# Performance work log

Measured on AMD Instinct MI355X. Metric: run time of the kernel, lower is better.

## Reference

```python
import jax, jax.numpy as jnp
import numpy as np

KSIZE = 11
SIGMA = 1.5
WEIGHTS = (0.0448, 0.2856, 0.3001, 0.2363, 0.1333)  # Wang et al. 2003
K1, K2 = 0.01, 0.03
DATA_RANGE = 1.0


def _gaussian_kernel():
    x = jnp.arange(KSIZE, dtype=jnp.float32) - KSIZE // 2
    k = jnp.exp(-x ** 2 / (2.0 * SIGMA ** 2))
    return k / k.sum()


def _filt(x, k1d):
    # Depthwise 2D Gaussian as two separable 1D depthwise convs (outer-product
    # kernel + zero padding => identical to the torch 2D conv with padding=5).
    C = x.shape[1]
    pad = KSIZE // 2
    dn = ('NCHW', 'OIHW', 'NCHW')
    kh = jnp.tile(k1d.reshape(1, 1, KSIZE, 1), (C, 1, 1, 1))
    kw = jnp.tile(k1d.reshape(1, 1, 1, KSIZE), (C, 1, 1, 1))
    x = jax.lax.conv_general_dilated(x, kh, (1, 1), [(pad, pad), (0, 0)],
                                     dimension_numbers=dn, feature_group_count=C)
    x = jax.lax.conv_general_dilated(x, kw, (1, 1), [(0, 0), (pad, pad)],
                                     dimension_numbers=dn, feature_group_count=C)
    return x


def _ssim_per_channel(img1, img2, k1d):
    C1 = (K1 * DATA_RANGE) ** 2
    C2 = (K2 * DATA_RANGE) ** 2
    mu1 = _filt(img1, k1d)
    mu2 = _filt(img2, k1d)
    mu1_sq = mu1 * mu1
    mu2_sq = mu2 * mu2
    mu12 = mu1 * mu2
    sigma1_sq = _filt(img1 * img1, k1d) - mu1_sq
    sigma2_sq = _filt(img2 * img2, k1d) - mu2_sq
    sigma12 = _filt(img1 * img2, k1d) - mu12
    cs_map = (2.0 * sigma12 + C2) / (sigma1_sq + sigma2_sq + C2)
    ssim_map = (2.0 * mu12 + C1) / (mu1_sq + mu2_sq + C1) * cs_map
    return ssim_map.mean(axis=(2, 3)), cs_map.mean(axis=(2, 3))  # (B, C) each


def _avg_pool2(x):
    B, C, H, W = x.shape
    return x.reshape(B, C, H // 2, 2, W // 2, 2).mean(axis=(3, 5))


def setup_inputs() -> dict:
    key = jax.random.key(0)
    k1, k2 = jax.random.split(key)
    img1 = jax.random.uniform(k1, (16, 3, 512, 512), dtype=jnp.float32)
    img2 = jax.random.uniform(k2, (16, 3, 512, 512), dtype=jnp.float32)
    return {"img1": img1, "img2": img2}


def reference(img1, img2):
    weights = jnp.array(WEIGHTS, dtype=jnp.float32)
    k1d = _gaussian_kernel()
    x1 = img1.astype(jnp.float32)
    x2 = img2.astype(jnp.float32)
    levels = len(WEIGHTS)
    mcs = []
    for i in range(levels):
        ssim_c, cs_c = _ssim_per_channel(x1, x2, k1d)
        if i < levels - 1:
            mcs.append(cs_c.mean(axis=1))
            x1 = _avg_pool2(x1)
            x2 = _avg_pool2(x2)
        else:
            mcs.append(ssim_c.mean(axis=1))
    mcs = jnp.clip(jnp.stack(mcs, axis=1), 0.0, None)  # (B, levels)
    ms_ssim_val = (mcs ** weights[None, :]).prod(axis=1)  # (B,)
    return ms_ssim_val.mean()
```

## Files before the change

### kernel.cpp

```cpp
#include <hip/hip_runtime.h>

#define NT 256

typedef float v2f __attribute__((ext_vector_type(2)));
typedef float f4u __attribute__((ext_vector_type(4), aligned(4)));

__device__ __forceinline__ constexpr float Wj(int j) {
    return (j < 0 || j > 10) ? 0.f :
           (j == 0 || j == 10) ? 0.00102838f :
           (j == 1 || j == 9)  ? 0.00759878f :
           (j == 2 || j == 8)  ? 0.03600077f :
           (j == 3 || j == 7)  ? 0.10936069f :
           (j == 4 || j == 6)  ? 0.21300553f : 0.26601172f;
}

__global__ __attribute__((amdgpu_flat_work_group_size(NT, NT), amdgpu_waves_per_eu(2, 4)))
void msssim_slide_kernel(
    const float* __restrict__ x1, const float* __restrict__ x2, int strideIn,
    float* __restrict__ p1, float* __restrict__ p2, int strideOut,
    float* __restrict__ accCS, float* __restrict__ accSSIM,
    int H, int W, int strips, int chunksY, int chunkRows, int padded)
{
    const int t = threadIdx.x;
    const int lane = t & 63;

    const int cpx = gridDim.x >> 3;
    const int lb = (blockIdx.x & 7) * cpx + (blockIdx.x >> 3);
    const int wid = lb * (NT / 64) + (t >> 6);

    const int perImg = strips * chunksY;
    const int img = wid / perImg;
    const int rem = wid - img * perImg;
    const int strip = rem / chunksY;
    const int chunk = rem % chunksY;
    const int cc = strip * 64 + lane;
    const int r0 = chunk * chunkRows;
    const int hEnd = r0 + chunkRows + 5;
    const bool edge = (!padded) && (strip == 0 || strip == strips - 1);
    const bool laneValid = (cc < W);
    const bool doPool = (p1 != nullptr);
    const int Wp = W >> 1;

    const size_t imgIn = (size_t)img * H * strideIn;
    const float* __restrict__ base1 = x1 + imgIn;
    const float* __restrict__ base2 = x2 + imgIn;
    const size_t imgOut = doPool ? (size_t)img * (H >> 1) * strideOut : 0;
    float* __restrict__ q1 = doPool ? (p1 + imgOut) : nullptr;
    float* __restrict__ q2 = doPool ? (p2 + imgOut) : nullptr;

    float nx1[12], nx2[12];
    v2f psd[11], psq[11];
    float prs1 = 0.f, prs2 = 0.f;
    float cs_s = 0.f, ssim_s = 0.f;

    auto loadRow = [&](int h) {
        if (h < 0 || h >= H || !laneValid) return;
        const float* __restrict__ r1 = base1 + (size_t)h * strideIn;
        const float* __restrict__ r2 = base2 + (size_t)h * strideIn;
        if (!edge) {
            const f4u* a4 = reinterpret_cast<const f4u*>(r1 + (cc - 5));
            const f4u* b4 = reinterpret_cast<const f4u*>(r2 + (cc - 5));
            f4u A0 = a4[0], A1 = a4[1], A2 = a4[2];
            f4u B0 = b4[0], B1 = b4[1], B2 = b4[2];
#pragma unroll
            for (int j = 0; j < 4; ++j) { nx1[j] = A0[j]; nx1[4 + j] = A1[j]; nx1[8 + j] = A2[j]; }
#pragma unroll
            for (int j = 0; j < 4; ++j) { nx2[j] = B0[j]; nx2[4 + j] = B1[j]; nx2[8 + j] = B2[j]; }
        } else {
#pragma unroll
            for (int j = 0; j < 12; ++j) {
                int col = cc + j - 5;
                int cl = col < 0 ? 0 : (col > W - 1 ? W - 1 : col);
                float a = r1[cl], b = r2[cl];
                bool ok = (col >= 0) && (col < W);
                nx1[j] = ok ? a : 0.f;
                nx2[j] = ok ? b : 0.f;
            }
        }
    };

    loadRow(r0 - 5);

    const float C1 = 0.0001f, C2 = 0.0009f;

    for (int hb = r0 - 5; hb < hEnd; hb += 11) {
#pragma unroll
        for (int p = 0; p < 11; ++p) {
            const int h = hb + p;
            if (h < hEnd) {
                v2f acc_sd = (v2f){0.f, 0.f}, acc_sq = (v2f){0.f, 0.f};
                const bool rv = (h >= 0) && (h < H);
                if (rv) {
                    if (doPool && h >= r0 && h < r0 + chunkRows) {
                        float ra = nx1[5] + nx1[6];
                        float rb = nx2[5] + nx2[6];
                        if ((h & 1) == 0) { prs1 = ra; prs2 = rb; }
                        else if (!(lane & 1) && laneValid) {
                            size_t po = (size_t)(h >> 1) * strideOut + (cc >> 1);
                            q1[po] = 0.25f * (prs1 + ra);
                            q2[po] = 0.25f * (prs2 + rb);
                            if (cc == 0) {
                                *(f4u*)&q1[po - 8] = (f4u){0.f, 0.f, 0.f, 0.f};
                                *(f4u*)&q1[po - 4] = (f4u){0.f, 0.f, 0.f, 0.f};
                                *(f4u*)&q2[po - 8] = (f4u){0.f, 0.f, 0.f, 0.f};
                                *(f4u*)&q2[po - 4] = (f4u){0.f, 0.f, 0.f, 0.f};
                            }
                            if ((cc >> 1) == Wp - 1) {
#pragma unroll
                                for (int j = 1; j <= 8; ++j) { q1[po + j] = 0.f; q2[po + j] = 0.f; }
                            }
                        }
                    }
#pragma unroll
                    for (int j = 0; j < 11; ++j) {
                        float s = nx1[j] + nx2[j];
                        float d = nx1[j] - nx2[j];
                        v2f sd = {s, d};
                        v2f w2 = {Wj(j), Wj(j)};
                        acc_sd = __builtin_elementwise_fma(w2, sd, acc_sd);
                        acc_sq = __builtin_elementwise_fma(w2, sd * sd, acc_sq);
                    }
                }
                if (h + 1 < hEnd) loadRow(h + 1);
                __builtin_amdgcn_sched_barrier(0);
#pragma unroll
                for (int k = 0; k < 11; ++k) {
                    const int slot = (p + 5 - k + 11) % 11;
                    v2f w2 = {Wj(k), Wj(k)};
                    if (k == 0) {
                        psd[slot] = w2 * acc_sd;
                        psq[slot] = w2 * acc_sq;
                    } else {
                        psd[slot] = __builtin_elementwise_fma(w2, acc_sd, psd[slot]);
                        psq[slot] = __builtin_elementwise_fma(w2, acc_sq, psq[slot]);
                    }
                }
                const int o = h - 5;
                if (o >= r0) {
                    const int es = (p + 6) % 11;
                    v2f m2 = psd[es] * psd[es];
                    v2f t1 = psq[es] - m2;
                    float num_cs = 0.5f * (t1.x - t1.y) + C2;
                    float den_cs = 0.5f * (t1.x + t1.y) + C2;
                    float num_ss = 0.5f * (m2.x - m2.y) + C1;
                    float den_ss = 0.5f * (m2.x + m2.y) + C1;
                    float cs = num_cs / den_cs;
                    float ss = num_ss * cs / den_ss;
                    if (laneValid) { cs_s += cs; ssim_s += ss; }
                }
            }
        }
    }

#pragma unroll
    for (int off = 32; off > 0; off >>= 1) {
        cs_s += __shfl_down(cs_s, off);
        ssim_s += __shfl_down(ssim_s, off);
    }
    if (lane == 0) {
        atomicAdd(&accCS[img], cs_s);
        atomicAdd(&accSSIM[img], ssim_s);
    }
}

__global__ void finalize_kernel(const float* __restrict__ acc, float* __restrict__ out) {
    __shared__ float vals[16];
    int t = threadIdx.x;
    if (t < 16) {
        const float w[5] = {0.0448f, 0.2856f, 0.3001f, 0.2363f, 0.1333f};
        float v = 1.f;
#pragma unroll
        for (int l = 0; l < 5; ++l) {
            int Hl = 512 >> l;
            float denom = 3.f * (float)Hl * (float)Hl;
            const float* src = (l < 4) ? (acc + l * 48) : (acc + 256 + l * 48);
            float m = src[3 * t] + src[3 * t + 1] + src[3 * t + 2];
            m = m / denom;
            m = fmaxf(m, 0.f);
            v *= powf(m, w[l]);
        }
        vals[t] = v;
    }
    __syncthreads();
    if (t == 0) {
        float s = 0.f;
        for (int i = 0; i < 16; ++i) s += vals[i];
        out[0] = s / 16.f;
    }
}

extern "C" void kernel_launch(void* const* d_in, const int* in_sizes, int n_in,
                              void* d_out, int out_size, void* d_ws, size_t ws_size,
                              hipStream_t stream) {
    const float* img1 = (const float*)d_in[0];
    const float* img2 = (const float*)d_in[1];
    float* out = (float*)d_out;
    float* ws = (float*)d_ws;

    float* acc = ws;
    size_t off = 512;

    float* a1[5];
    float* a2[5];
    int strideL[5];
    a1[0] = (float*)img1; a2[0] = (float*)img2; strideL[0] = 512;
    for (int l = 1; l < 5; ++l) {
        int Hl = 512 >> l;
        strideL[l] = Hl + 16;
        a1[l] = ws + off + 8; off += (size_t)48 * Hl * strideL[l];
    }
    for (int l = 1; l < 5; ++l) {
        int Hl = 512 >> l;
        a2[l] = ws + off + 8; off += (size_t)48 * Hl * strideL[l];
    }

    hipMemsetAsync(acc, 0, 512 * sizeof(float), stream);

    for (int l = 0; l < 5; ++l) {
        int Hl = 512 >> l;
        int strips = (Hl + 63) / 64;
        int chunkRows = (l == 0) ? 64 : (l == 1 ? 16 : 8);
        int chunksY = Hl / chunkRows;
        int waves = 48 * strips * chunksY;
        int blocks = waves / (NT / 64);
        float* pp1 = (l < 4) ? a1[l + 1] : nullptr;
        float* pp2 = (l < 4) ? a2[l + 1] : nullptr;
        int so = (l < 4) ? strideL[l + 1] : 0;
        msssim_slide_kernel<<<blocks, NT, 0, stream>>>(
            a1[l], a2[l], strideL[l], pp1, pp2, so,
            acc + l * 48, acc + 256 + l * 48,
            Hl, Hl, strips, chunksY, chunkRows, l > 0 ? 1 : 0);
    }
    finalize_kernel<<<1, 64, 0, stream>>>(acc, out);
}
```

Measured before the change: 199.4 us.

## Double-buffer row loads two rows ahead and pack sum/diff via packed FMA

Row registers become two buffers that alternate, and each row is now fetched two iterations before it is used, so global load latency has more compute to hide behind. The loop is unrolled to 22 rows to keep the ring-slot indices compile-time constant, and the sched_barrier is removed so the compiler can interleave loads with arithmetic. The sum and difference pair is now computed with one packed FMA. The cost is more register pressure and a larger unrolled body, which may lower occupancy.

```diff
diff --git a/kernel.cpp b/kernel.cpp
--- a/kernel.cpp
+++ b/kernel.cpp
@@ -48,12 +48,12 @@
     float* __restrict__ q1 = doPool ? (p1 + imgOut) : nullptr;
     float* __restrict__ q2 = doPool ? (p2 + imgOut) : nullptr;
 
-    float nx1[12], nx2[12];
+    float nA1[12], nA2[12], nB1[12], nB2[12];
     v2f psd[11], psq[11];
     float prs1 = 0.f, prs2 = 0.f;
     float cs_s = 0.f, ssim_s = 0.f;
 
-    auto loadRow = [&](int h) {
+    auto loadRow = [&](int h, float (&d1)[12], float (&d2)[12]) {
         if (h < 0 || h >= H || !laneValid) return;
         const float* __restrict__ r1 = base1 + (size_t)h * strideIn;
         const float* __restrict__ r2 = base2 + (size_t)h * strideIn;
@@ -63,9 +63,9 @@
             f4u A0 = a4[0], A1 = a4[1], A2 = a4[2];
             f4u B0 = b4[0], B1 = b4[1], B2 = b4[2];
 #pragma unroll
-            for (int j = 0; j < 4; ++j) { nx1[j] = A0[j]; nx1[4 + j] = A1[j]; nx1[8 + j] = A2[j]; }
-#pragma unroll
-            for (int j = 0; j < 4; ++j) { nx2[j] = B0[j]; nx2[4 + j] = B1[j]; nx2[8 + j] = B2[j]; }
+            for (int j = 0; j < 4; ++j) { d1[j] = A0[j]; d1[4 + j] = A1[j]; d1[8 + j] = A2[j]; }
+#pragma unroll
+            for (int j = 0; j < 4; ++j) { d2[j] = B0[j]; d2[4 + j] = B1[j]; d2[8 + j] = B2[j]; }
         } else {
 #pragma unroll
             for (int j = 0; j < 12; ++j) {
@@ -73,27 +73,32 @@
                 int cl = col < 0 ? 0 : (col > W - 1 ? W - 1 : col);
                 float a = r1[cl], b = r2[cl];
                 bool ok = (col >= 0) && (col < W);
-                nx1[j] = ok ? a : 0.f;
-                nx2[j] = ok ? b : 0.f;
+                d1[j] = ok ? a : 0.f;
+                d2[j] = ok ? b : 0.f;
             }
         }
     };
 
-    loadRow(r0 - 5);
+    loadRow(r0 - 5, nA1, nA2);
+    loadRow(r0 - 4, nB1, nB2);
 
     const float C1 = 0.0001f, C2 = 0.0009f;
 
-    for (int hb = r0 - 5; hb < hEnd; hb += 11) {
-#pragma unroll
-        for (int p = 0; p < 11; ++p) {
-            const int h = hb + p;
+    for (int hb = r0 - 5; hb < hEnd; hb += 22) {
+#pragma unroll
+        for (int pp = 0; pp < 22; ++pp) {
+            const int h = hb + pp;
             if (h < hEnd) {
+                const int p = pp % 11;
+                float (&x1w)[12] = (pp & 1) ? nB1 : nA1;
+                float (&x2w)[12] = (pp & 1) ? nB2 : nA2;
+
                 v2f acc_sd = (v2f){0.f, 0.f}, acc_sq = (v2f){0.f, 0.f};
                 const bool rv = (h >= 0) && (h < H);
                 if (rv) {
                     if (doPool && h >= r0 && h < r0 + chunkRows) {
-                        float ra = nx1[5] + nx1[6];
-                        float rb = nx2[5] + nx2[6];
+                        float ra = x1w[5] + x1w[6];
+                        float rb = x2w[5] + x2w[6];
                         if ((h & 1) == 0) { prs1 = ra; prs2 = rb; }
                         else if (!(lane & 1) && laneValid) {
                             size_t po = (size_t)(h >> 1) * strideOut + (cc >> 1);
@@ -113,16 +118,15 @@
                     }
 #pragma unroll
                     for (int j = 0; j < 11; ++j) {
-                        float s = nx1[j] + nx2[j];
-                        float d = nx1[j] - nx2[j];
-                        v2f sd = {s, d};
+                        v2f xx1 = {x1w[j], x1w[j]};
+                        v2f xx2 = {x2w[j], x2w[j]};
+                        v2f sd = __builtin_elementwise_fma((v2f){1.f, -1.f}, xx2, xx1);
                         v2f w2 = {Wj(j), Wj(j)};
                         acc_sd = __builtin_elementwise_fma(w2, sd, acc_sd);
                         acc_sq = __builtin_elementwise_fma(w2, sd * sd, acc_sq);
                     }
                 }
-                if (h + 1 < hEnd) loadRow(h + 1);
-                __builtin_amdgcn_sched_barrier(0);
+                if (h + 2 < hEnd) loadRow(h + 2, x1w, x2w);
 #pragma unroll
                 for (int k = 0; k < 11; ++k) {
                     const int slot = (p + 5 - k + 11) % 11;
```

Result: slower. 250.9 us (+25.8%).
